# Performance work log

Hardware: AMD Instinct MI355X
Metric: run time of the kernel (lower is better)

The kernel has to match this reference:

```python
import jax, jax.numpy as jnp
import numpy as np

HEADS = 16
HEAD_DIM = 64
EMBED = HEADS * HEAD_DIM  # 1024
B, S = 2, 2048


def setup_inputs() -> dict:
    key = jax.random.key(0)
    ks = jax.random.split(key, 9)
    return {
        "value": jax.random.normal(ks[0], (B, S, EMBED), dtype=jnp.float32),
        "key": jax.random.normal(ks[1], (B, S, EMBED), dtype=jnp.float32),
        "query": jax.random.normal(ks[2], (B, S, EMBED), dtype=jnp.float32),
        "mask": jax.random.randint(ks[3], (B, 1, S, S), 0, 2, dtype=jnp.int32),
        "Wq": jax.random.normal(ks[4], (HEAD_DIM, HEAD_DIM), dtype=jnp.float32) * 0.02,
        "Wk": jax.random.normal(ks[5], (HEAD_DIM, HEAD_DIM), dtype=jnp.float32) * 0.02,
        "Wv": jax.random.normal(ks[6], (HEAD_DIM, HEAD_DIM), dtype=jnp.float32) * 0.02,
        "Wo": jax.random.normal(ks[7], (EMBED, EMBED), dtype=jnp.float32) * 0.02,
        "bo": jnp.zeros((EMBED,), dtype=jnp.float32),
    }


def reference(value, key, query, mask, Wq, Wk, Wv, Wo, bo):
    N, Lv = value.shape[0], value.shape[1]
    Lk, Lq = key.shape[1], query.shape[1]
    # Faithful to original: plain reshape (N, heads, len, head_dim), NOT transpose.
    v = value.reshape(N, HEADS, Lv, HEAD_DIM)
    k = key.reshape(N, HEADS, Lk, HEAD_DIM)
    q = query.reshape(N, HEADS, Lq, HEAD_DIM)
    # Per-head Linear (no bias): x @ W.T
    V = jnp.einsum('bhld,ed->bhle', v, Wv)
    K = jnp.einsum('bhld,ed->bhle', k, Wk)
    Q = jnp.einsum('bhld,ed->bhle', q, Wq)
    score = jnp.einsum('bhqd,bhkd->bhqk', Q, K)  # [B,H,Sq,Sk]
    score = jnp.where(mask == 0, jnp.float32(-1e20), score)
    # Faithful quirk: scale by sqrt(embed_size), not sqrt(head_dim)
    scale = jnp.float32(EMBED ** 0.5)
    attn = jax.nn.softmax(score / scale, axis=3)
    out = jnp.einsum('bhqk,bhkd->bhqd', attn, V).reshape(N, Lq, HEADS * HEAD_DIM)
    return out @ Wo.T + bo
```

## Files before the change

kernel.cpp:

```cpp
#include <hip/hip_runtime.h>
#include <hip/hip_bf16.h>
#include <cstdint>
#include <cstddef>

#define S_LEN 2048
#define N_HEADS 16
#define HD 64
#define EMB 1024
#define N_BATCH 2
#define N_BH (N_BATCH * N_HEADS)

typedef __attribute__((ext_vector_type(4))) float f32x4;
typedef __attribute__((ext_vector_type(8))) short short8;
typedef __attribute__((ext_vector_type(8))) _Float16 half8;
typedef __attribute__((ext_vector_type(2))) unsigned uint2v;
typedef __attribute__((ext_vector_type(4))) unsigned uint4v;

__device__ __forceinline__ f32x4 mfma16h(half8 a, half8 b, f32x4 c) {
    return __builtin_amdgcn_mfma_f32_16x16x32_f16(a, b, c, 0, 0, 0);
}

__device__ __forceinline__ unsigned pkh(float a, float b) {
    return __builtin_bit_cast(unsigned, __builtin_amdgcn_cvt_pkrtz(a, b));
}

#if __has_builtin(__builtin_amdgcn_exp2f)
__device__ __forceinline__ float fast_exp2(float x) { return __builtin_amdgcn_exp2f(x); }
#else
__device__ __forceinline__ float fast_exp2(float x) { return exp2f(x); }
#endif

__device__ __forceinline__ void gl2lds16(const short* g, short* l) {
    __builtin_amdgcn_global_load_lds(
        (const __attribute__((address_space(1))) void*)g,
        (__attribute__((address_space(3))) void*)l, 16, 0, 0);
}

__global__ __launch_bounds__(256) void prep_kernel(
    const float* __restrict__ q_in, const float* __restrict__ k_in,
    const float* __restrict__ v_in,
    const float* __restrict__ Wq, const float* __restrict__ Wk,
    const float* __restrict__ Wv, const float* __restrict__ Wo,
    const int* __restrict__ mask,
    short* __restrict__ Qb, short* __restrict__ Kb, short* __restrict__ Vt,
    short* __restrict__ Woh, unsigned long long* __restrict__ bits) {
    __shared__ short Al[64 * 72];
    __shared__ short Wl[64 * 72];
    __shared__ short Ol[64 * 72];
    int bx = blockIdx.x;
    int t = threadIdx.x;

    if (bx >= 3072) {
        if (bx < 11264) {
            int wid = ((bx - 3072) * 256 + t) >> 6;
            int lane = t & 63;
            const int* src = mask + (size_t)wid * 256 + lane;
            unsigned long long w0 = __ballot(src[0] != 0);
            unsigned long long w1 = __ballot(src[64] != 0);
            unsigned long long w2 = __ballot(src[128] != 0);
            unsigned long long w3 = __ballot(src[192] != 0);
            if (lane == 0) {
                unsigned long long* dst = bits + (size_t)wid * 4;
                dst[0] = w0; dst[1] = w1; dst[2] = w2; dst[3] = w3;
            }
        } else {
            int i = (bx - 11264) * 256 + t;
            f32x4 a = reinterpret_cast<const f32x4*>(Wo)[i * 2];
            f32x4 b = reinterpret_cast<const f32x4*>(Wo)[i * 2 + 1];
            uint4 u = { pkh(a.x, a.y), pkh(a.z, a.w), pkh(b.x, b.y), pkh(b.z, b.w) };
            reinterpret_cast<uint4*>(Woh)[i] = u;
        }
        return;
    }

    int rt = bx & 31;
    int bh = (bx >> 5) & 31;
    int tz = bx >> 10;
    const float* src = (tz == 0 ? q_in : tz == 1 ? k_in : v_in)
                       + (size_t)bh * S_LEN * HD + (size_t)rt * 64 * HD;
    const float* W = (tz == 0 ? Wq : tz == 1 ? Wk : Wv);

#pragma unroll
    for (int r = 0; r < 4; r++) {
        int f4 = t + 256 * r;
        int row = f4 >> 4;
        int c4 = (f4 & 15) * 4;
        f32x4 a = reinterpret_cast<const f32x4*>(src)[f4];
        uint2 ua = { pkh(a.x, a.y), pkh(a.z, a.w) };
        *reinterpret_cast<uint2*>(&Al[row * 72 + c4]) = ua;
        f32x4 w = reinterpret_cast<const f32x4*>(W)[f4];
        uint2 uw = { pkh(w.x, w.y), pkh(w.z, w.w) };
        *reinterpret_cast<uint2*>(&Wl[row * 72 + c4]) = uw;
    }
    __syncthreads();

    int wave = t >> 6, lane = t & 63, quad = lane >> 4, col = lane & 15;
    half8 a0 = *reinterpret_cast<const half8*>(&Al[(wave * 16 + col) * 72 + quad * 8]);
    half8 a1 = *reinterpret_cast<const half8*>(&Al[(wave * 16 + col) * 72 + 32 + quad * 8]);

    const float C1 = 0.04508422002777448f;
    float scl = (tz == 0) ? C1 : 1.0f;

    f32x4 acc[4];
#pragma unroll
    for (int jt = 0; jt < 4; jt++) {
        half8 b0 = *reinterpret_cast<const half8*>(&Wl[(jt * 16 + col) * 72 + quad * 8]);
        half8 b1 = *reinterpret_cast<const half8*>(&Wl[(jt * 16 + col) * 72 + 32 + quad * 8]);
        f32x4 c = {0.f, 0.f, 0.f, 0.f};
        c = mfma16h(a0, b0, c);
        c = mfma16h(a1, b1, c);
        acc[jt] = c;
    }
    __syncthreads();

    if (tz < 2) {
#pragma unroll
        for (int jt = 0; jt < 4; jt++)
#pragma unroll
            for (int i = 0; i < 4; i++)
                Ol[(wave * 16 + quad * 4 + i) * 72 + jt * 16 + col] =
                    __builtin_bit_cast(short, (_Float16)(acc[jt][i] * scl));
        __syncthreads();
        short* dst = (tz == 0 ? Qb : Kb) + (size_t)bh * S_LEN * HD + (size_t)rt * 64 * HD;
        int row = t >> 2, ck = (t & 3) * 16;
        short8 o0 = *reinterpret_cast<const short8*>(&Ol[row * 72 + ck]);
        short8 o1 = *reinterpret_cast<const short8*>(&Ol[row * 72 + ck + 8]);
        *reinterpret_cast<short8*>(&dst[row * 64 + ck]) = o0;
        *reinterpret_cast<short8*>(&dst[row * 64 + ck + 8]) = o1;
    } else {
#pragma unroll
        for (int jt = 0; jt < 4; jt++)
#pragma unroll
            for (int i = 0; i < 4; i++)
                Ol[(jt * 16 + col) * 72 + wave * 16 + quad * 4 + i] =
                    __builtin_bit_cast(short, (_Float16)acc[jt][i]);
        __syncthreads();
        short* dst = Vt + (size_t)bh * HD * S_LEN + rt * 64;
        int d = t >> 2, ck = (t & 3) * 16;
        short8 o0 = *reinterpret_cast<const short8*>(&Ol[d * 72 + ck]);
        short8 o1 = *reinterpret_cast<const short8*>(&Ol[d * 72 + ck + 8]);
        uint4v u0 = __builtin_bit_cast(uint4v, o0);
        uint4v u1 = __builtin_bit_cast(uint4v, o1);
        short8 n0 = __builtin_bit_cast(short8, (uint4v){u0.x, u0.y, u1.x, u1.y});
        short8 n1 = __builtin_bit_cast(short8, (uint4v){u0.z, u0.w, u1.z, u1.w});
        *reinterpret_cast<short8*>(&dst[(size_t)d * S_LEN + ck]) = n0;
        *reinterpret_cast<short8*>(&dst[(size_t)d * S_LEN + ck + 8]) = n1;
    }
}

__global__ __launch_bounds__(512, 4) void attn_kernel(
    const short* __restrict__ Qb, const short* __restrict__ Kb,
    const short* __restrict__ Vt, const unsigned long long* __restrict__ mbits,
    short* __restrict__ Xb) {
    int qt = blockIdx.x;
    int bh = blockIdx.y;
    int b = bh >> 4;
    int t = threadIdx.x, wave = t >> 6, lane = t & 63, quad = lane >> 4, col = lane & 15;
    int qg = wave & 3;
    int par = wave >> 2;

    __shared__ short smem[32768];

    const short* Qh = Qb + (size_t)bh * S_LEN * HD;
    const short* Kh = Kb + (size_t)bh * S_LEN * HD;
    const short* Vh = Vt + (size_t)bh * HD * S_LEN;
    int q0 = qt * 128 + qg * 32;

    half8 qf00 = *reinterpret_cast<const half8*>(&Qh[(size_t)(q0 + col) * HD + quad * 8]);
    half8 qf01 = *reinterpret_cast<const half8*>(&Qh[(size_t)(q0 + col) * HD + 32 + quad * 8]);
    half8 qf10 = *reinterpret_cast<const half8*>(&Qh[(size_t)(q0 + 16 + col) * HD + quad * 8]);
    half8 qf11 = *reinterpret_cast<const half8*>(&Qh[(size_t)(q0 + 16 + col) * HD + 32 + quad * 8]);

    const unsigned long long* mrow0 = mbits + (size_t)(b * S_LEN + q0 + col) * 32;
    const unsigned long long* mrow1 = mbits + (size_t)(b * S_LEN + q0 + 16 + col) * 32;

    int lrow = lane >> 3;
    int lsw = (lane & 7) ^ lrow;
    int grow = wave * 8 + lrow;
    const short* kp0 = Kh + grow * 64 + lsw * 8;
    const short* vp0 = Vh + (size_t)grow * S_LEN + lsw * 8;
    short* kl0 = smem + wave * 512;
    short* kl1 = smem + 8192 + wave * 512;
    short* vl0 = smem + 16384 + wave * 512;
    short* vl1 = smem + 24576 + wave * 512;

    gl2lds16(kp0, kl0);
    gl2lds16(kp0 + 4096, kl1);
    gl2lds16(vp0, vl0);
    gl2lds16(vp0 + 64, vl1);

    unsigned bs[4];
#pragma unroll
    for (int i = 0; i < 4; i++) bs[i] = 1u << (quad * 4 + i);
    half8 ones = { (_Float16)1.f, (_Float16)1.f, (_Float16)1.f, (_Float16)1.f,
                   (_Float16)1.f, (_Float16)1.f, (_Float16)1.f, (_Float16)1.f };

    int sw = quad ^ (col & 7);
    unsigned long long mw0 = mrow0[par];
    unsigned long long mw1 = mrow1[par];

    f32x4 o[4][2];
    f32x4 l0 = {0.f, 0.f, 0.f, 0.f}, l1 = {0.f, 0.f, 0.f, 0.f};
#pragma unroll
    for (int dt = 0; dt < 4; dt++) {
        o[dt][0] = (f32x4){0.f, 0.f, 0.f, 0.f};
        o[dt][1] = (f32x4){0.f, 0.f, 0.f, 0.f};
    }
    __syncthreads();

    for (int s = 0; s < 16; s++) {
        int rd = (s & 1) * 4096;
        int wr = 4096 - rd;
        unsigned long long mn0, mn1;
        if (s < 15) {
            const short* ka = kp0 + (2 * s + 2) * 4096;
            const short* va = vp0 + (2 * s + 2) * 64;
            gl2lds16(ka, kl0 + wr);
            gl2lds16(ka + 4096, kl1 + wr);
            gl2lds16(va, vl0 + wr);
            gl2lds16(va + 64, vl1 + wr);
            mn0 = mrow0[2 * s + 2 + par];
            mn1 = mrow1[2 * s + 2 + par];
        }
        const short* Kp = smem + par * 8192 + rd;
        const short* Vp = smem + 16384 + par * 8192 + rd;
        unsigned wA[4][2], wB[4][2];
#pragma unroll
        for (int mt = 0; mt < 4; mt++) {
            const short* kbase = &Kp[(mt * 16 + col) * 64];
            half8 ka0 = *reinterpret_cast<const half8*>(&kbase[sw * 8]);
            half8 ka1 = *reinterpret_cast<const half8*>(&kbase[(sw ^ 4) * 8]);
            f32x4 c0 = {0.f, 0.f, 0.f, 0.f};
            f32x4 c1 = {0.f, 0.f, 0.f, 0.f};
            c0 = mfma16h(ka0, qf00, c0);
            c0 = mfma16h(ka1, qf01, c0);
            c1 = mfma16h(ka0, qf10, c1);
            c1 = mfma16h(ka1, qf11, c1);
            unsigned g0 = (unsigned)(mw0 >> (mt * 16));
            unsigned g1 = (unsigned)(mw1 >> (mt * 16));
            float p00 = fast_exp2((g0 & bs[0]) ? c0[0] : -200.0f);
            float p01 = fast_exp2((g0 & bs[1]) ? c0[1] : -200.0f);
            float p02 = fast_exp2((g0 & bs[2]) ? c0[2] : -200.0f);
            float p03 = fast_exp2((g0 & bs[3]) ? c0[3] : -200.0f);
            wA[mt][0] = pkh(p00, p01);
            wA[mt][1] = pkh(p02, p03);
            float p10 = fast_exp2((g1 & bs[0]) ? c1[0] : -200.0f);
            float p11 = fast_exp2((g1 & bs[1]) ? c1[1] : -200.0f);
            float p12 = fast_exp2((g1 & bs[2]) ? c1[2] : -200.0f);
            float p13 = fast_exp2((g1 & bs[3]) ? c1[3] : -200.0f);
            wB[mt][0] = pkh(p10, p11);
            wB[mt][1] = pkh(p12, p13);
        }
#pragma unroll
        for (int c = 0; c < 2; c++) {
            auto ra0 = __builtin_amdgcn_permlane32_swap(wA[2 * c][0], wA[2 * c + 1][0], false, false);
            auto ra1 = __builtin_amdgcn_permlane32_swap(wA[2 * c][1], wA[2 * c + 1][1], false, false);
            auto rb0 = __builtin_amdgcn_permlane32_swap(wB[2 * c][0], wB[2 * c + 1][0], false, false);
            auto rb1 = __builtin_amdgcn_permlane32_swap(wB[2 * c][1], wB[2 * c + 1][1], false, false);
            half8 pb0 = __builtin_bit_cast(half8, (uint4v){ra0[0], ra1[0], ra0[1], ra1[1]});
            half8 pb1 = __builtin_bit_cast(half8, (uint4v){rb0[0], rb1[0], rb0[1], rb1[1]});
            l0 = mfma16h(ones, pb0, l0);
            l1 = mfma16h(ones, pb1, l1);
#pragma unroll
            for (int dt = 0; dt < 4; dt++) {
                half8 va = *reinterpret_cast<const half8*>(
                    &Vp[(dt * 16 + col) * 64 + (((c * 4 + quad) ^ (col & 7)) * 8)]);
                o[dt][0] = mfma16h(va, pb0, o[dt][0]);
                o[dt][1] = mfma16h(va, pb1, o[dt][1]);
            }
        }
        if (s < 15) {
            mw0 = mn0;
            mw1 = mn1;
        }
        __syncthreads();
    }

    float* Obuf = (float*)smem;
    short* Ps = smem + 16384;
    float* Lbuf = (float*)(smem + 25600);
    if (par == 1) {
        float* ob = Obuf + qg * 2048 + lane * 32;
#pragma unroll
        for (int dt = 0; dt < 4; dt++) {
            *reinterpret_cast<f32x4*>(&ob[((dt * 2 + 0) ^ (lane & 7)) * 4]) = o[dt][0];
            *reinterpret_cast<f32x4*>(&ob[((dt * 2 + 1) ^ (lane & 7)) * 4]) = o[dt][1];
        }
        if (quad == 0) {
            Lbuf[qg * 32 + col] = l0[0];
            Lbuf[qg * 32 + 16 + col] = l1[0];
        }
    }
    __syncthreads();
    if (par == 0) {
        short* Pw = Ps + qg * (32 * 72);
        float* ob = Obuf + qg * 2048 + lane * 32;
        float inv0 = 1.0f / (l0[0] + Lbuf[qg * 32 + col]);
        float inv1 = 1.0f / (l1[0] + Lbuf[qg * 32 + 16 + col]);
#pragma unroll
        for (int dt = 0; dt < 4; dt++) {
            f32x4 a0 = *reinterpret_cast<const f32x4*>(&ob[((dt * 2 + 0) ^ (lane & 7)) * 4]);
            f32x4 a1 = *reinterpret_cast<const f32x4*>(&ob[((dt * 2 + 1) ^ (lane & 7)) * 4]);
            float v00 = (o[dt][0][0] + a0.x) * inv0, v01 = (o[dt][0][1] + a0.y) * inv0;
            float v02 = (o[dt][0][2] + a0.z) * inv0, v03 = (o[dt][0][3] + a0.w) * inv0;
            float v10 = (o[dt][1][0] + a1.x) * inv1, v11 = (o[dt][1][1] + a1.y) * inv1;
            float v12 = (o[dt][1][2] + a1.z) * inv1, v13 = (o[dt][1][3] + a1.w) * inv1;
            uint2 dw0 = { pkh(v00, v01), pkh(v02, v03) };
            uint2 dw1 = { pkh(v10, v11), pkh(v12, v13) };
            *reinterpret_cast<uint2*>(&Pw[col * 72 + dt * 16 + quad * 4]) = dw0;
            *reinterpret_cast<uint2*>(&Pw[(16 + col) * 72 + dt * 16 + quad * 4]) = dw1;
        }
        int rr = lane >> 2, ckk = (lane & 3) * 16;
        short* Xrow = Xb + (size_t)bh * S_LEN * HD + (size_t)(q0 + rr) * HD;
        short8 x0 = *reinterpret_cast<const short8*>(&Pw[rr * 72 + ckk]);
        short8 x1 = *reinterpret_cast<const short8*>(&Pw[rr * 72 + ckk + 8]);
        *reinterpret_cast<short8*>(&Xrow[ckk]) = x0;
        *reinterpret_cast<short8*>(&Xrow[ckk + 8]) = x1;
        short* Xrow2 = Xrow + 16 * HD;
        short8 y0 = *reinterpret_cast<const short8*>(&Pw[(16 + rr) * 72 + ckk]);
        short8 y1 = *reinterpret_cast<const short8*>(&Pw[(16 + rr) * 72 + ckk + 8]);
        *reinterpret_cast<short8*>(&Xrow2[ckk]) = y0;
        *reinterpret_cast<short8*>(&Xrow2[ckk + 8]) = y1;
    }
}

__global__ __launch_bounds__(256, 4) void final_kernel(
    const short* __restrict__ Xb, const short* __restrict__ Woh,
    const float* __restrict__ bo, float* __restrict__ out) {
    int nb = blockIdx.x;
    int mb = blockIdx.y;
    int t = threadIdx.x, wave = t >> 6, lane = t & 63, quad = lane >> 4, col = lane & 15;
    __shared__ short Xs[128 * 64];
    __shared__ short Ws[64 * 64];

    int m0 = mb * 128, n0 = nb * 64;
    int r0 = t >> 3, cc = t & 7;

    int dstX[4], dstW[2];
    const short* xg[4];
    const short* wg[2];
#pragma unroll
    for (int u = 0; u < 4; u++) {
        int row = r0 + u * 32;
        dstX[u] = row * 64 + ((cc ^ (row & 7)) * 8);
        xg[u] = Xb + (size_t)(m0 + row) * EMB + cc * 8;
    }
#pragma unroll
    for (int u = 0; u < 2; u++) {
        int row = r0 + u * 32;
        dstW[u] = row * 64 + ((cc ^ (row & 7)) * 8);
        wg[u] = Woh + (size_t)(n0 + row) * EMB + cc * 8;
    }

    short8 px[4], pw[2];
#pragma unroll
    for (int u = 0; u < 4; u++) px[u] = *reinterpret_cast<const short8*>(xg[u]);
#pragma unroll
    for (int u = 0; u < 2; u++) pw[u] = *reinterpret_cast<const short8*>(wg[u]);
#pragma unroll
    for (int u = 0; u < 4; u++) *reinterpret_cast<short8*>(&Xs[dstX[u]]) = px[u];
#pragma unroll
    for (int u = 0; u < 2; u++) *reinterpret_cast<short8*>(&Ws[dstW[u]]) = pw[u];
    __syncthreads();

    int sw = quad ^ (col & 7);
    f32x4 acc[2][4];
#pragma unroll
    for (int mf = 0; mf < 2; mf++)
#pragma unroll
        for (int nf = 0; nf < 4; nf++) acc[mf][nf] = (f32x4){0.f, 0.f, 0.f, 0.f};

    for (int s = 0; s < 16; s++) {
        if (s < 15) {
#pragma unroll
            for (int u = 0; u < 4; u++)
                px[u] = *reinterpret_cast<const short8*>(xg[u] + (s + 1) * 64);
#pragma unroll
            for (int u = 0; u < 2; u++)
                pw[u] = *reinterpret_cast<const short8*>(wg[u] + (s + 1) * 64);
        }
        const short* ar0 = &Xs[(wave * 32 + col) * 64];
        const short* ar1 = &Xs[(wave * 32 + 16 + col) * 64];
        half8 a00 = *reinterpret_cast<const half8*>(&ar0[sw * 8]);
        half8 a01 = *reinterpret_cast<const half8*>(&ar0[(sw ^ 4) * 8]);
        half8 a10 = *reinterpret_cast<const half8*>(&ar1[sw * 8]);
        half8 a11 = *reinterpret_cast<const half8*>(&ar1[(sw ^ 4) * 8]);
#pragma unroll
        for (int nf = 0; nf < 4; nf++) {
            const short* br = &Ws[(nf * 16 + col) * 64];
            half8 b0 = *reinterpret_cast<const half8*>(&br[sw * 8]);
            half8 b1 = *reinterpret_cast<const half8*>(&br[(sw ^ 4) * 8]);
            acc[0][nf] = mfma16h(a00, b0, acc[0][nf]);
            acc[0][nf] = mfma16h(a01, b1, acc[0][nf]);
            acc[1][nf] = mfma16h(a10, b0, acc[1][nf]);
            acc[1][nf] = mfma16h(a11, b1, acc[1][nf]);
        }
        __syncthreads();
        if (s < 15) {
#pragma unroll
            for (int u = 0; u < 4; u++) *reinterpret_cast<short8*>(&Xs[dstX[u]]) = px[u];
#pragma unroll
            for (int u = 0; u < 2; u++) *reinterpret_cast<short8*>(&Ws[dstW[u]]) = pw[u];
            __syncthreads();
        }
    }

    float bb[4];
#pragma unroll
    for (int nf = 0; nf < 4; nf++) bb[nf] = bo[n0 + nf * 16 + col];
#pragma unroll
    for (int mf = 0; mf < 2; mf++)
#pragma unroll
        for (int i = 0; i < 4; i++) {
            int row = m0 + wave * 32 + mf * 16 + quad * 4 + i;
            float* orow = out + (size_t)row * EMB + n0;
#pragma unroll
            for (int nf = 0; nf < 4; nf++)
                orow[nf * 16 + col] = acc[mf][nf][i] + bb[nf];
        }
}

extern "C" void kernel_launch(void* const* d_in, const int* in_sizes, int n_in,
                              void* d_out, int out_size, void* d_ws, size_t ws_size,
                              hipStream_t stream) {
    const float* value = (const float*)d_in[0];
    const float* key_  = (const float*)d_in[1];
    const float* query = (const float*)d_in[2];
    const int*   mask  = (const int*)d_in[3];
    const float* Wq = (const float*)d_in[4];
    const float* Wk = (const float*)d_in[5];
    const float* Wv = (const float*)d_in[6];
    const float* Wo = (const float*)d_in[7];
    const float* bo = (const float*)d_in[8];
    float* out = (float*)d_out;

    char* ws = (char*)d_ws;
    short* Qb  = (short*)(ws);
    short* Kb  = (short*)(ws + (size_t)8  * 1048576);
    short* Vt  = (short*)(ws + (size_t)16 * 1048576);
    short* Xb  = (short*)(ws + (size_t)24 * 1048576);
    short* Woh = (short*)(ws + (size_t)32 * 1048576);
    unsigned long long* mbits =
        (unsigned long long*)(ws + (size_t)34 * 1048576);

    prep_kernel<<<dim3(3072 + 8192 + 512), dim3(256), 0, stream>>>(
        query, key_, value, Wq, Wk, Wv, Wo, mask, Qb, Kb, Vt, Woh, mbits);
    attn_kernel<<<dim3(S_LEN / 128, N_BH), dim3(512), 0, stream>>>(Qb, Kb, Vt, mbits, Xb);
    final_kernel<<<dim3(EMB / 64, (N_BATCH * S_LEN) / 128), dim3(256), 0, stream>>>(
        Xb, Woh, bo, out);
}
```

Measured before the change: 193.9 us.

## Double-buffer output projection GEMM with direct global-to-LDS loads

The final projection GEMM now loads X and Wo tiles straight from global memory into LDS, instead of staging them through registers and storing them with separate LDS writes. It also double-buffers the LDS tiles, so only one barrier per k-step is needed and the next tile's fetch overlaps the current tile's MFMAs. The XOR swizzle is moved onto the global address so the LDS layout stays compatible with the existing read pattern. The LDS footprint grows to 64KB per block, which may lower the achievable occupancy.

After: 193.6 us. Within noise of the previous version (-0.1%).

```diff
diff --git a/kernel.cpp b/kernel.cpp
--- a/kernel.cpp
+++ b/kernel.cpp
@@ -330,38 +330,23 @@
     int nb = blockIdx.x;
     int mb = blockIdx.y;
     int t = threadIdx.x, wave = t >> 6, lane = t & 63, quad = lane >> 4, col = lane & 15;
-    __shared__ short Xs[128 * 64];
-    __shared__ short Ws[64 * 64];
+    __shared__ short smem[32768];
 
     int m0 = mb * 128, n0 = nb * 64;
-    int r0 = t >> 3, cc = t & 7;
-
-    int dstX[4], dstW[2];
-    const short* xg[4];
-    const short* wg[2];
-#pragma unroll
-    for (int u = 0; u < 4; u++) {
-        int row = r0 + u * 32;
-        dstX[u] = row * 64 + ((cc ^ (row & 7)) * 8);
-        xg[u] = Xb + (size_t)(m0 + row) * EMB + cc * 8;
-    }
-#pragma unroll
-    for (int u = 0; u < 2; u++) {
-        int row = r0 + u * 32;
-        dstW[u] = row * 64 + ((cc ^ (row & 7)) * 8);
-        wg[u] = Woh + (size_t)(n0 + row) * EMB + cc * 8;
-    }
-
-    short8 px[4], pw[2];
-#pragma unroll
-    for (int u = 0; u < 4; u++) px[u] = *reinterpret_cast<const short8*>(xg[u]);
-#pragma unroll
-    for (int u = 0; u < 2; u++) pw[u] = *reinterpret_cast<const short8*>(wg[u]);
-#pragma unroll
-    for (int u = 0; u < 4; u++) *reinterpret_cast<short8*>(&Xs[dstX[u]]) = px[u];
-#pragma unroll
-    for (int u = 0; u < 2; u++) *reinterpret_cast<short8*>(&Ws[dstW[u]]) = pw[u];
-    __syncthreads();
+
+    int lrow = lane >> 3;
+    int lsw = (lane & 7) ^ lrow;
+    const short* xg = Xb + (size_t)(m0 + wave * 8 + lrow) * EMB + lsw * 8;
+    const short* wg = Woh + (size_t)(n0 + wave * 8 + lrow) * EMB + lsw * 8;
+    short* xl = smem + wave * 512;
+    short* wl = smem + 16384 + wave * 512;
+
+    gl2lds16(xg, xl);
+    gl2lds16(xg + 32 * EMB, xl + 2048);
+    gl2lds16(xg + 64 * EMB, xl + 4096);
+    gl2lds16(xg + 96 * EMB, xl + 6144);
+    gl2lds16(wg, wl);
+    gl2lds16(wg + 32 * EMB, wl + 2048);
 
     int sw = quad ^ (col & 7);
     f32x4 acc[2][4];
@@ -369,25 +354,32 @@
     for (int mf = 0; mf < 2; mf++)
 #pragma unroll
         for (int nf = 0; nf < 4; nf++) acc[mf][nf] = (f32x4){0.f, 0.f, 0.f, 0.f};
+    __syncthreads();
 
     for (int s = 0; s < 16; s++) {
+        int rd = (s & 1) << 13;
+        int wr = 8192 - rd;
         if (s < 15) {
-#pragma unroll
-            for (int u = 0; u < 4; u++)
-                px[u] = *reinterpret_cast<const short8*>(xg[u] + (s + 1) * 64);
-#pragma unroll
-            for (int u = 0; u < 2; u++)
-                pw[u] = *reinterpret_cast<const short8*>(wg[u] + (s + 1) * 64);
-        }
-        const short* ar0 = &Xs[(wave * 32 + col) * 64];
-        const short* ar1 = &Xs[(wave * 32 + 16 + col) * 64];
+            const short* xs = xg + (s + 1) * 64;
+            const short* ws2 = wg + (s + 1) * 64;
+            gl2lds16(xs, xl + wr);
+            gl2lds16(xs + 32 * EMB, xl + wr + 2048);
+            gl2lds16(xs + 64 * EMB, xl + wr + 4096);
+            gl2lds16(xs + 96 * EMB, xl + wr + 6144);
+            gl2lds16(ws2, wl + wr);
+            gl2lds16(ws2 + 32 * EMB, wl + wr + 2048);
+        }
+        const short* Xp = smem + rd;
+        const short* Wp = smem + 16384 + rd;
+        const short* ar0 = &Xp[(wave * 32 + col) * 64];
+        const short* ar1 = &Xp[(wave * 32 + 16 + col) * 64];
         half8 a00 = *reinterpret_cast<const half8*>(&ar0[sw * 8]);
         half8 a01 = *reinterpret_cast<const half8*>(&ar0[(sw ^ 4) * 8]);
         half8 a10 = *reinterpret_cast<const half8*>(&ar1[sw * 8]);
         half8 a11 = *reinterpret_cast<const half8*>(&ar1[(sw ^ 4) * 8]);
 #pragma unroll
         for (int nf = 0; nf < 4; nf++) {
-            const short* br = &Ws[(nf * 16 + col) * 64];
+            const short* br = &Wp[(nf * 16 + col) * 64];
             half8 b0 = *reinterpret_cast<const half8*>(&br[sw * 8]);
             half8 b1 = *reinterpret_cast<const half8*>(&br[(sw ^ 4) * 8]);
             acc[0][nf] = mfma16h(a00, b0, acc[0][nf]);
@@ -396,13 +388,6 @@
             acc[1][nf] = mfma16h(a11, b1, acc[1][nf]);
         }
         __syncthreads();
-        if (s < 15) {
-#pragma unroll
-            for (int u = 0; u < 4; u++) *reinterpret_cast<short8*>(&Xs[dstX[u]]) = px[u];
-#pragma unroll
-            for (int u = 0; u < 2; u++) *reinterpret_cast<short8*>(&Ws[dstW[u]]) = pw[u];
-            __syncthreads();
-        }
     }
 
     float bb[4];
```
